# Kernel optimization log

Hardware: AMD Instinct MI355X
Metric: run time of the kernel (lower is better)

Reference implementation:

```python
import jax, jax.numpy as jnp
import numpy as np
from jax import lax

STRIDE = 16
ANCHOR_BASE = 16
PRE_NMS = 6000
POST_NMS = 2000
NMS_THRESH = 0.7


def _generate_anchors(base_size=16, ratios=(0.5, 1.0, 2.0), scales=(8, 16, 32)):
    w = h = float(base_size)
    x_ctr = 0.5 * (w - 1)
    y_ctr = 0.5 * (h - 1)
    size = w * h
    anchors = []
    for r in ratios:
        ws = np.round(np.sqrt(size / r))
        hs = np.round(ws * r)
        for s in scales:
            wss, hss = ws * s, hs * s
            anchors.append([x_ctr - 0.5 * (wss - 1), y_ctr - 0.5 * (hss - 1),
                            x_ctr + 0.5 * (wss - 1), y_ctr + 0.5 * (hss - 1)])
    return np.array(anchors, dtype=np.float32)  # [9,4]


def _all_anchors(width, height, stride):
    base = _generate_anchors(ANCHOR_BASE)  # [A,4]
    sx = np.arange(width, dtype=np.float32) * stride
    gy, gx = np.meshgrid(np.arange(height, dtype=np.float32) * stride, sx, indexing='ij')
    shifts = np.stack([gx.ravel(), gy.ravel(), gx.ravel(), gy.ravel()], axis=1)  # [K,4] h-major
    return jnp.asarray((shifts[:, None, :] + base[None, :, :]).reshape(-1, 4))  # [K*A,4]


def setup_inputs() -> dict:
    key = jax.random.key(0)
    k1, k2 = jax.random.split(key)
    H = W = 64
    bbox_deltas = jax.random.normal(k1, (1, 36, H, W), dtype=jnp.float32)
    scores = jax.random.uniform(k2, (1, 2, 9 * H, W), dtype=jnp.float32)
    return {"bbox_deltas": bbox_deltas, "scores": scores, "im_w": 1024, "im_h": 1024}


def reference(bbox_deltas, scores, im_w, im_h):
    H, W = bbox_deltas.shape[2], bbox_deltas.shape[3]
    # fg scores: reshape [1,2,9H,W] -> [1,18,H,W], take channels 9:18
    sc = scores.reshape(1, 18, H, W)[:, 9:, :, :].transpose(0, 2, 3, 1).reshape(-1)
    dl = bbox_deltas.transpose(0, 2, 3, 1).reshape(-1, 4)
    anchors = _all_anchors(W, H, STRIDE)

    # bbox_transform_inv (decode)
    aw = anchors[:, 2] - anchors[:, 0] + 1.0
    ah = anchors[:, 3] - anchors[:, 1] + 1.0
    acx = anchors[:, 0] + 0.5 * aw
    acy = anchors[:, 1] + 0.5 * ah
    pcx = dl[:, 0] * aw + acx
    pcy = dl[:, 1] * ah + acy
    pw = jnp.exp(dl[:, 2]) * aw
    ph = jnp.exp(dl[:, 3]) * ah
    x1 = jnp.clip(pcx - 0.5 * pw, 0.0, im_w - 1.0)
    y1 = jnp.clip(pcy - 0.5 * ph, 0.0, im_h - 1.0)
    x2 = jnp.clip(pcx + 0.5 * pw, 0.0, im_w - 1.0)
    y2 = jnp.clip(pcy + 0.5 * ph, 0.0, im_h - 1.0)
    props = jnp.stack([x1, y1, x2, y2], axis=1)

    # min-size filter
    thresh = 16.0 * (float(im_h) / float(im_w))
    keep_f = ((x2 - x1 + 1.0) >= thresh) & ((y2 - y1 + 1.0) >= thresh)
    sc_m = jnp.where(keep_f, sc, -jnp.inf)

    # pre-NMS top-k by score
    top_sc, idx = lax.top_k(sc_m, PRE_NMS)
    top_p = props[idx]  # [PRE_NMS,4], sorted by score desc
    valid = jnp.isfinite(top_sc)

    # pairwise IoU (with +1 box convention, as in py_cpu_nms)
    bx1, by1, bx2, by2 = top_p[:, 0], top_p[:, 1], top_p[:, 2], top_p[:, 3]
    areas = (bx2 - bx1 + 1.0) * (by2 - by1 + 1.0)
    iw = jnp.maximum(jnp.minimum(bx2[:, None], bx2[None, :]) - jnp.maximum(bx1[:, None], bx1[None, :]) + 1.0, 0.0)
    ih = jnp.maximum(jnp.minimum(by2[:, None], by2[None, :]) - jnp.maximum(by1[:, None], by1[None, :]) + 1.0, 0.0)
    inter = iw * ih
    iou = inter / (areas[:, None] + areas[None, :] - inter)
    sup = iou > NMS_THRESH  # [N,N]

    ar = jnp.arange(PRE_NMS)

    def body(i, keep):
        row = sup[i] & keep[i] & (ar > i)
        return keep & (~row)

    keep = lax.fori_loop(0, PRE_NMS, body, valid)

    # take first POST_NMS kept (in score order), scatter into fixed-size output
    rank = jnp.cumsum(keep.astype(jnp.int32)) - 1
    sel = keep & (rank < POST_NMS)
    dst = jnp.where(sel, rank, POST_NMS)  # invalid rows dumped into slot POST_NMS
    out_b = jnp.zeros((POST_NMS + 1, 4), dtype=jnp.float32).at[dst].set(
        jnp.where(sel[:, None], top_p, 0.0))[:POST_NMS]
    out_s = jnp.zeros((POST_NMS + 1,), dtype=jnp.float32).at[dst].set(
        jnp.where(sel, top_sc, 0.0))[:POST_NMS]
    blob = jnp.concatenate([jnp.zeros((POST_NMS, 1), dtype=jnp.float32), out_b], axis=1)
    return blob, out_s[:, None]
```

## Files before the change

### kernel.cpp

```cpp
#include <hip/hip_runtime.h>
#include <math.h>

typedef unsigned int u32;
typedef unsigned long long u64;

#define NANCH   36864
#define PRE     6000
#define POST    2000
#define NWORDS  94

#define OFF_PROPS   ((size_t)0)
#define OFF_SV      ((size_t)589824)
#define OFF_SORTED  ((size_t)884736)
#define OFF_SEL     ((size_t)932864)
#define OFF_MASK    ((size_t)1227776)
#define OFF_CTRL    ((size_t)5739776)
#define OFF_H1      ((size_t)5740032)
#define OFF_INVALW  ((size_t)5744384)
#define OFF_KEEPW   ((size_t)5745152)
#define ZERO_BYTES  ((size_t)(256 + 4352 + 768))

__device__ __constant__ float BA[9][4] = {
  {-84.f,-40.f,99.f,55.f},   {-176.f,-88.f,191.f,103.f}, {-360.f,-184.f,375.f,199.f},
  {-56.f,-56.f,71.f,71.f},   {-120.f,-120.f,135.f,135.f},{-248.f,-248.f,263.f,263.f},
  {-36.f,-80.f,51.f,95.f},   {-80.f,-168.f,95.f,183.f},  {-168.f,-344.f,183.f,359.f}};

__device__ __forceinline__ u32 key_bin(u32 key) {
  if (key < 0xBF000000u) return 0u;
  u32 b = ((key >> 13) - 0x5F800u) + 1u;
  return b > 1024u ? 1024u : b;
}

__global__ void decode_k(const float* __restrict__ deltas, const float* __restrict__ scores,
                         const int* __restrict__ imw_p, const int* __restrict__ imh_p,
                         float4* __restrict__ props, u64* __restrict__ sortvals,
                         u32* __restrict__ h1) {
  #pragma clang fp contract(off)
  int i = blockIdx.x * 256 + threadIdx.x;
  if (i >= NANCH) return;
  int a = i % 9;
  int pix = i / 9;
  int x = pix & 63, y = pix >> 6;

  float sc = scores[(9 + a) * 4096 + pix];
  float d0 = deltas[(a * 4 + 0) * 4096 + pix];
  float d1 = deltas[(a * 4 + 1) * 4096 + pix];
  float d2 = deltas[(a * 4 + 2) * 4096 + pix];
  float d3 = deltas[(a * 4 + 3) * 4096 + pix];

  float gx = (float)(x * 16), gy = (float)(y * 16);
  float ax1 = gx + BA[a][0], ay1 = gy + BA[a][1];
  float ax2 = gx + BA[a][2], ay2 = gy + BA[a][3];
  float aw = ax2 - ax1 + 1.0f, ah = ay2 - ay1 + 1.0f;
  float acx = ax1 + 0.5f * aw, acy = ay1 + 0.5f * ah;

  float pcx = d0 * aw + acx;
  float pcy = d1 * ah + acy;
  float pw = (float)exp((double)d2) * aw;
  float ph = (float)exp((double)d3) * ah;

  float imw1 = (float)imw_p[0] - 1.0f, imh1 = (float)imh_p[0] - 1.0f;
  float x1 = fminf(fmaxf(pcx - 0.5f * pw, 0.0f), imw1);
  float y1 = fminf(fmaxf(pcy - 0.5f * ph, 0.0f), imh1);
  float x2 = fminf(fmaxf(pcx + 0.5f * pw, 0.0f), imw1);
  float y2 = fminf(fmaxf(pcy + 0.5f * ph, 0.0f), imh1);
  props[i] = make_float4(x1, y1, x2, y2);

  float thresh = 16.0f * ((float)imh_p[0] / (float)imw_p[0]);
  bool keep = (x2 - x1 + 1.0f >= thresh) && (y2 - y1 + 1.0f >= thresh);
  u32 key = keep ? (__float_as_uint(sc) | 0x80000000u) : 0u;
  sortvals[i] = ((u64)key << 32) | (u64)(0xFFFFFFFFu - (u32)i);
  u32 bin = key_bin(key);
  if (bin) atomicAdd(&h1[bin], 1u);
}

__global__ void scan_k(const u32* __restrict__ h1, u32* __restrict__ ctrl) {
  int l = threadIdx.x;
  u32 loc[16], suf[16];
  #pragma unroll
  for (int k = 0; k < 16; ++k) loc[k] = h1[1 + l * 16 + k];
  u32 acc = 0;
  #pragma unroll
  for (int k = 15; k >= 0; --k) { acc += loc[k]; suf[k] = acc; }
  u32 sfx = acc;
  for (int off = 1; off < 64; off <<= 1) {
    u32 o = __shfl_down(sfx, off);
    if (l + off < 64) sfx += o;
  }
  u32 S_above = sfx - acc;
  u64 mball = __ballot(suf[0] + S_above >= (u32)PRE);
  if (mball == 0ULL) { if (l == 0) ctrl[0] = 0u; return; }
  int L = 63 - __builtin_clzll(mball);
  if (l == L) {
    int kk = 0;
    for (int k = 15; k >= 0; --k)
      if (suf[k] + S_above >= (u32)PRE) { kk = k; break; }
    ctrl[0] = (u32)(1 + 16 * L + kk);
  }
}

__global__ void compact_k(const u64* __restrict__ sv, u32* __restrict__ ctrl,
                          u64* __restrict__ sel) {
  int i = blockIdx.x * 256 + threadIdx.x;
  if (i >= NANCH) return;
  u32 chosen = ctrl[0];
  u64 v = sv[i];
  if (key_bin((u32)(v >> 32)) >= chosen) {
    u32 p = atomicAdd(&ctrl[6], 1u);
    sel[p] = v;
  }
}

__global__ void rank_k(const u64* __restrict__ sel, const u32* __restrict__ ctrl,
                       u64* __restrict__ sorted, u64* __restrict__ invalw) {
  __shared__ u64 sj[256];
  u32 n = ctrl[6];
  int i = blockIdx.x * 256 + threadIdx.x;
  if ((u32)(blockIdx.x * 256) >= n) return;
  u64 vi = ((u32)i < n) ? sel[i] : 0ULL;
  u32 cnt = 0;
  for (u32 jb = 0; jb < n; jb += 256) {
    __syncthreads();
    if (jb + threadIdx.x < n) sj[threadIdx.x] = sel[jb + threadIdx.x];
    __syncthreads();
    u32 m = min(256u, n - jb);
    #pragma unroll 8
    for (u32 j = 0; j < m; ++j) cnt += (u32)(sj[j] > vi);
  }
  if ((u32)i < n && cnt < (u32)PRE) {
    sorted[cnt] = vi;
    if ((u32)(vi >> 32) == 0u)
      atomicOr((unsigned long long*)&invalw[cnt >> 6], 1ULL << (cnt & 63));
  }
}

__global__ void mask_k(const u64* __restrict__ sorted, const float4* __restrict__ props,
                       u64* __restrict__ mask) {
  #pragma clang fp contract(off)
  __shared__ float4 cb[64];
  int jb = blockIdx.x;
  if (jb < (int)blockIdx.y) return;
  int i = blockIdx.y * 64 + threadIdx.x;
  int jj = jb * 64 + threadIdx.x;
  float4 cc = make_float4(0.f, 0.f, 0.f, 0.f);
  if (jj < PRE) {
    u64 v = sorted[jj];
    cc = props[0xFFFFu - ((u32)v & 0xFFFFu)];
  }
  cb[threadIdx.x] = cc;
  __syncthreads();
  if (i >= PRE) return;
  u64 vi = sorted[i];
  float4 b = props[0xFFFFu - ((u32)vi & 0xFFFFu)];
  float ai = (b.z - b.x + 1.0f) * (b.w - b.y + 1.0f);
  u64 bits = 0ULL;
  int jmax = min(64, PRE - jb * 64);
  for (int j = 0; j < jmax; ++j) {
    float4 c = cb[j];
    float aj = (c.z - c.x + 1.0f) * (c.w - c.y + 1.0f);
    float iw = fmaxf(fminf(b.z, c.z) - fmaxf(b.x, c.x) + 1.0f, 0.0f);
    float ih = fmaxf(fminf(b.w, c.w) - fmaxf(b.y, c.y) + 1.0f, 0.0f);
    float inter = iw * ih;
    float iou = inter / (ai + aj - inter);
    bits |= ((u64)(iou > 0.7f)) << j;
  }
  mask[(size_t)i * NWORDS + jb] = bits;
}

__device__ __forceinline__ u64 rl64(u64 v, int lane) {
  u32 lo = (u32)__builtin_amdgcn_readlane((int)(u32)v, lane);
  u32 hi = (u32)__builtin_amdgcn_readlane((int)(u32)(v >> 32), lane);
  return ((u64)hi << 32) | (u64)lo;
}
__device__ __forceinline__ u64 rfl64(u64 v) {
  u32 lo = (u32)__builtin_amdgcn_readfirstlane((int)(u32)v);
  u32 hi = (u32)__builtin_amdgcn_readfirstlane((int)(u32)(v >> 32));
  return ((u64)hi << 32) | (u64)lo;
}

__global__ void __launch_bounds__(1024) nms_scan_k(const u64* __restrict__ mask,
                                                   const u64* __restrict__ invalw,
                                                   u64* __restrict__ keepw) {
  __shared__ u64 Lrem[NWORDS];
  __shared__ u64 Ldiag[64];
  __shared__ u64 Lkeep;
  __shared__ int Lstop;
  __shared__ int Llast;
  const int t = threadIdx.x;
  const int g = t >> 7;
  const int w = t & 127;
  const bool loader = (w < NWORDS);
  if (t < NWORDS) Lrem[t] = invalw[t];
  if (t == 0) { Lstop = 0; Llast = NWORDS - 1; }
  u64 rv = 0;
  u64 B0[8], B1[8], B2[8];
  int kept = 0;
  __syncthreads();

#define ISSUE(bb, BUF) \
  if ((bb) < NWORDS && loader) { \
    u64 st_ = Lrem[(bb)]; \
    const int row0_ = (bb) * 64 + g * 8; \
    const u64* pp_ = mask + (size_t)row0_ * NWORDS + w; \
    _Pragma("unroll") \
    for (int j = 0; j < 8; ++j) { \
      bool ok_ = (w >= (bb)) && (row0_ + j < PRE) && !((st_ >> (g * 8 + j)) & 1ULL); \
      BUF[j] = ok_ ? pp_[(size_t)j * NWORDS] : 0ULL; \
    } \
  }

#define STEP(bb, BUF) { \
    if (w == (bb)) {                      \
      atomicOr((u32*)&Lrem[(bb)], (u32)rv); \
      atomicOr(((u32*)&Lrem[(bb)]) + 1, (u32)(rv >> 32)); \
      _Pragma("unroll") \
      for (int j = 0; j < 8; ++j) Ldiag[g * 8 + j] = BUF[j]; \
    } \
    if ((bb) + 3 < NWORDS && w == (bb) + 3) {   \
      atomicOr((u32*)&Lrem[(bb) + 3], (u32)rv); \
      atomicOr(((u32*)&Lrem[(bb) + 3]) + 1, (u32)(rv >> 32)); \
    } \
    __syncthreads();                      \
    if (t < 64) { \
      u64 dgl = Ldiag[t]; \
      u64 avail = ~rfl64(Lrem[(bb)]);     \
      u64 kb = 0; \
      while (avail) { \
        int i_ = __builtin_ctzll(avail); \
        kb |= 1ULL << i_; \
        u64 di_ = rl64(dgl, i_); \
        avail &= ~di_ & ~((2ULL << i_) - 1ULL);  \
      } \
      if (t == 0) { \
        keepw[(bb)] = kb; \
        Lkeep = kb; \
        kept += (int)__popcll(kb); \
        if (kept >= POST) { Lstop = 1; Llast = (bb); } \
      } \
    } \
    __syncthreads();                      \
    { \
      u64 kb_ = Lkeep; \
      const int base_ = g * 8; \
      _Pragma("unroll") \
      for (int j = 0; j < 8; ++j) { \
        u64 k_ = (kb_ >> (base_ + j)) & 1ULL; \
        rv |= (0ULL - k_) & BUF[j]; \
      } \
    } \
    ISSUE((bb) + 3, BUF)                  \
    if (Lstop) break; }

  ISSUE(0, B0)
  ISSUE(1, B1)
  ISSUE(2, B2)
  for (int bb = 0; bb < NWORDS; bb += 3) {
    STEP(bb, B0)
    if (bb + 1 < NWORDS) STEP(bb + 1, B1)
    if (bb + 2 < NWORDS) STEP(bb + 2, B2)
  }
#undef ISSUE
#undef STEP

  __syncthreads();
  int last = Llast;
  for (int w2 = t; w2 < NWORDS; w2 += 1024)
    if (w2 > last) keepw[w2] = 0ULL;
}

__global__ void outscatter_k(const u64* __restrict__ keepw, const u64* __restrict__ sorted,
                             const float4* __restrict__ props, float* __restrict__ out) {
  __shared__ u64 wl[NWORDS];
  __shared__ u32 pre[NWORDS];
  int t = threadIdx.x;
  for (int i = t; i < 12000; i += 1024) out[i] = 0.0f;
  if (t < NWORDS) wl[t] = keepw[t];
  __syncthreads();
  if (t == 0) {
    u32 run = 0;
    for (int w = 0; w < NWORDS; ++w) { pre[w] = run; run += (u32)__popcll(wl[w]); }
  }
  __syncthreads();
  for (int i = t; i < PRE; i += 1024) {
    int w = i >> 6;
    u64 word = wl[w];
    if ((word >> (i & 63)) & 1ULL) {
      u32 rank = pre[w] + (u32)__popcll(word & ((1ULL << (i & 63)) - 1ULL));
      if (rank < POST) {
        u64 v = sorted[i];
        float4 b = props[0xFFFFu - ((u32)v & 0xFFFFu)];
        out[rank * 5 + 1] = b.x;
        out[rank * 5 + 2] = b.y;
        out[rank * 5 + 3] = b.z;
        out[rank * 5 + 4] = b.w;
        out[10000 + rank] = __uint_as_float((u32)(v >> 32) & 0x7FFFFFFFu);
      }
    }
  }
}

extern "C" void kernel_launch(void* const* d_in, const int* in_sizes, int n_in,
                              void* d_out, int out_size, void* d_ws, size_t ws_size,
                              hipStream_t stream) {
  const float* deltas = (const float*)d_in[0];
  const float* scores = (const float*)d_in[1];
  const int* imw = (const int*)d_in[2];
  const int* imh = (const int*)d_in[3];
  char* ws = (char*)d_ws;

  float4* props   = (float4*)(ws + OFF_PROPS);
  u64*    svals   = (u64*)(ws + OFF_SV);
  u64*    sorted  = (u64*)(ws + OFF_SORTED);
  u64*    sel     = (u64*)(ws + OFF_SEL);
  u64*    maskb   = (u64*)(ws + OFF_MASK);
  u32*    ctrl    = (u32*)(ws + OFF_CTRL);
  u32*    h1      = (u32*)(ws + OFF_H1);
  u64*    invalw  = (u64*)(ws + OFF_INVALW);
  u64*    keepw   = (u64*)(ws + OFF_KEEPW);

  hipMemsetAsync(ws + OFF_CTRL, 0, ZERO_BYTES, stream);

  decode_k<<<144, 256, 0, stream>>>(deltas, scores, imw, imh, props, svals, h1);
  scan_k<<<1, 64, 0, stream>>>(h1, ctrl);
  compact_k<<<144, 256, 0, stream>>>(svals, ctrl, sel);
  rank_k<<<144, 256, 0, stream>>>(sel, ctrl, sorted, invalw);

  dim3 mgrid(NWORDS, NWORDS);
  mask_k<<<mgrid, 64, 0, stream>>>(sorted, props, maskb);

  nms_scan_k<<<1, 1024, 0, stream>>>(maskb, invalw, keepw);
  outscatter_k<<<1, 1024, 0, stream>>>(keepw, sorted, props, (float*)d_out);
}
```

Measured before the change: 333.6 us.

## Process two NMS mask words per barrier step in serial scan

The block-wide NMS scan now resolves two 64-box words per step instead of one. It stages the diagonal and cross-block suppression tiles in shared memory and runs the second word's greedy loop using suppression bits from the first. This halves the number of __syncthreads round trips in the serial scan. In exchange it adds register pressure (four 8-entry buffers), a longer serial wavefront loop per step, and reduced lookahead depth, since prefetch is now two double-steps ahead.

```diff
diff --git a/kernel.cpp b/kernel.cpp
--- a/kernel.cpp
+++ b/kernel.cpp
@@ -8,6 +8,7 @@
 #define PRE     6000
 #define POST    2000
 #define NWORDS  94
+#define NSTEPS  47
 
 #define OFF_PROPS   ((size_t)0)
 #define OFF_SV      ((size_t)589824)
@@ -182,8 +183,10 @@
                                                    const u64* __restrict__ invalw,
                                                    u64* __restrict__ keepw) {
   __shared__ u64 Lrem[NWORDS];
-  __shared__ u64 Ldiag[64];
-  __shared__ u64 Lkeep;
+  __shared__ u64 LdAA[64];
+  __shared__ u64 LdAB[64];
+  __shared__ u64 LdBB[64];
+  __shared__ u64 LkeepA, LkeepB;
   __shared__ int Lstop;
   __shared__ int Llast;
   const int t = threadIdx.x;
@@ -193,74 +196,100 @@
   if (t < NWORDS) Lrem[t] = invalw[t];
   if (t == 0) { Lstop = 0; Llast = NWORDS - 1; }
   u64 rv = 0;
-  u64 B0[8], B1[8], B2[8];
+  u64 B0A[8], B0B[8], B1A[8], B1B[8];
   int kept = 0;
   __syncthreads();
 
-#define ISSUE(bb, BUF) \
-  if ((bb) < NWORDS && loader) { \
-    u64 st_ = Lrem[(bb)]; \
-    const int row0_ = (bb) * 64 + g * 8; \
-    const u64* pp_ = mask + (size_t)row0_ * NWORDS + w; \
+#define ISSUE2(ss, BA_, BB_) \
+  if ((ss) < NSTEPS && loader) { \
+    const int Ai_ = 2 * (ss), Bi_ = Ai_ + 1; \
+    u64 stA_ = Lrem[Ai_], stB_ = Lrem[Bi_]; \
+    const int rA_ = Ai_ * 64 + g * 8, rB_ = Bi_ * 64 + g * 8; \
+    const u64* pA_ = mask + (size_t)rA_ * NWORDS + w; \
+    const u64* pB_ = mask + (size_t)rB_ * NWORDS + w; \
     _Pragma("unroll") \
     for (int j = 0; j < 8; ++j) { \
-      bool ok_ = (w >= (bb)) && (row0_ + j < PRE) && !((st_ >> (g * 8 + j)) & 1ULL); \
-      BUF[j] = ok_ ? pp_[(size_t)j * NWORDS] : 0ULL; \
-    } \
-  }
-
-#define STEP(bb, BUF) { \
-    if (w == (bb)) {                      \
-      atomicOr((u32*)&Lrem[(bb)], (u32)rv); \
-      atomicOr(((u32*)&Lrem[(bb)]) + 1, (u32)(rv >> 32)); \
+      bool okA_ = (w >= Ai_) && !((stA_ >> (g * 8 + j)) & 1ULL); \
+      bool okB_ = (w >= Bi_) && (rB_ + j < PRE) && !((stB_ >> (g * 8 + j)) & 1ULL); \
+      BA_[j] = okA_ ? pA_[(size_t)j * NWORDS] : 0ULL; \
+      BB_[j] = okB_ ? pB_[(size_t)j * NWORDS] : 0ULL; \
+    } \
+  }
+
+#define STEP2(ss, BA_, BB_) { \
+    const int A_ = 2 * (ss), B_ = A_ + 1; \
+    if (w == A_ || w == B_) {             \
+      atomicOr((u32*)&Lrem[w], (u32)rv); \
+      atomicOr(((u32*)&Lrem[w]) + 1, (u32)(rv >> 32)); \
+    } \
+    if (w == A_) { \
       _Pragma("unroll") \
-      for (int j = 0; j < 8; ++j) Ldiag[g * 8 + j] = BUF[j]; \
-    } \
-    if ((bb) + 3 < NWORDS && w == (bb) + 3) {   \
-      atomicOr((u32*)&Lrem[(bb) + 3], (u32)rv); \
-      atomicOr(((u32*)&Lrem[(bb) + 3]) + 1, (u32)(rv >> 32)); \
-    } \
+      for (int j = 0; j < 8; ++j) LdAA[g * 8 + j] = BA_[j]; \
+    } \
+    if (w == B_) { \
+      _Pragma("unroll") \
+      for (int j = 0; j < 8; ++j) { LdAB[g * 8 + j] = BA_[j]; LdBB[g * 8 + j] = BB_[j]; } \
+    } \
+    { const int A2_ = A_ + 4;             \
+      if (A2_ < NWORDS && (w == A2_ || w == A2_ + 1)) { \
+        atomicOr((u32*)&Lrem[w], (u32)rv); \
+        atomicOr(((u32*)&Lrem[w]) + 1, (u32)(rv >> 32)); \
+      } } \
     __syncthreads();                      \
     if (t < 64) { \
-      u64 dgl = Ldiag[t]; \
-      u64 avail = ~rfl64(Lrem[(bb)]);     \
-      u64 kb = 0; \
-      while (avail) { \
-        int i_ = __builtin_ctzll(avail); \
-        kb |= 1ULL << i_; \
-        u64 di_ = rl64(dgl, i_); \
-        avail &= ~di_ & ~((2ULL << i_) - 1ULL);  \
+      u64 dAA = LdAA[t], dAB = LdAB[t], dBB = LdBB[t]; \
+      u64 availA = ~rfl64(Lrem[A_]); \
+      u64 kbA = 0, supB = 0; \
+      while (availA) { \
+        int i_ = __builtin_ctzll(availA); \
+        kbA |= 1ULL << i_; \
+        u64 rA1_ = rl64(dAA, i_); \
+        supB |= rl64(dAB, i_); \
+        availA &= ~rA1_ & ~((2ULL << i_) - 1ULL);  \
+      } \
+      u64 availB = ~(rfl64(Lrem[B_]) | supB); \
+      u64 kbB = 0; \
+      while (availB) { \
+        int i_ = __builtin_ctzll(availB); \
+        kbB |= 1ULL << i_; \
+        u64 rB1_ = rl64(dBB, i_); \
+        availB &= ~rB1_ & ~((2ULL << i_) - 1ULL); \
       } \
       if (t == 0) { \
-        keepw[(bb)] = kb; \
-        Lkeep = kb; \
-        kept += (int)__popcll(kb); \
-        if (kept >= POST) { Lstop = 1; Llast = (bb); } \
+        keepw[A_] = kbA; \
+        LkeepA = kbA; \
+        kept += (int)__popcll(kbA); \
+        if (kept >= POST) { Lstop = 1; Llast = A_; LkeepB = 0ULL; } \
+        else { \
+          keepw[B_] = kbB; \
+          LkeepB = kbB; \
+          kept += (int)__popcll(kbB); \
+          if (kept >= POST) { Lstop = 1; Llast = B_; } \
+        } \
       } \
     } \
     __syncthreads();                      \
     { \
-      u64 kb_ = Lkeep; \
+      u64 kA_ = LkeepA, kB_ = LkeepB; \
       const int base_ = g * 8; \
       _Pragma("unroll") \
       for (int j = 0; j < 8; ++j) { \
-        u64 k_ = (kb_ >> (base_ + j)) & 1ULL; \
-        rv |= (0ULL - k_) & BUF[j]; \
+        u64 mA_ = 0ULL - ((kA_ >> (base_ + j)) & 1ULL); \
+        u64 mB_ = 0ULL - ((kB_ >> (base_ + j)) & 1ULL); \
+        rv |= (mA_ & BA_[j]) | (mB_ & BB_[j]); \
       } \
     } \
-    ISSUE((bb) + 3, BUF)                  \
+    ISSUE2((ss) + 2, BA_, BB_)            \
     if (Lstop) break; }
 
-  ISSUE(0, B0)
-  ISSUE(1, B1)
-  ISSUE(2, B2)
-  for (int bb = 0; bb < NWORDS; bb += 3) {
-    STEP(bb, B0)
-    if (bb + 1 < NWORDS) STEP(bb + 1, B1)
-    if (bb + 2 < NWORDS) STEP(bb + 2, B2)
-  }
-#undef ISSUE
-#undef STEP
+  ISSUE2(0, B0A, B0B)
+  ISSUE2(1, B1A, B1B)
+  for (int s = 0; s < NSTEPS; s += 2) {
+    STEP2(s, B0A, B0B)
+    if (s + 1 < NSTEPS) STEP2(s + 1, B1A, B1B)
+  }
+#undef ISSUE2
+#undef STEP2
 
   __syncthreads();
   int last = Llast;
```

New measurement: 532.9 us. 1.6x slower.
